# Kernel tuning notes

Hardware: AMD Instinct MI355X
Metric: run time of the kernel (lower is better)

## Reference

```python
import jax, jax.numpy as jnp
import numpy as np

PRUNE_N, PRUNE_M = 2, 4
RIA_A = 1.0
NUM_HEADS = 16
HEAD_DIM = 128
ROPE_THETA = 10000.0


def sparse_mask(W, scaler_row, perm):
    # RIA metric: |W|/colsum + |W|/rowsum, scaled by sqrt(scaler_row)**a
    absW = jnp.abs(W)
    metric = (absW / absW.sum(axis=0, keepdims=True)
              + absW / absW.sum(axis=1, keepdims=True))
    metric = metric * (jnp.sqrt(scaler_row)[None, :] ** RIA_A)
    Wm = metric @ perm                      # permute columns: [R, C]
    R, C = Wm.shape
    nb = C // PRUNE_M
    blocks = Wm.reshape(R, nb, PRUNE_M)
    # hard N:M mask: top-n per block of m
    _, idx = jax.lax.top_k(blocks, PRUNE_N)           # [R, nb, n]
    hard = jax.nn.one_hot(idx, PRUNE_M, dtype=Wm.dtype).sum(axis=-2)  # [R, nb, m]
    soft = jax.nn.softmax(blocks, axis=-1)
    hard = hard.reshape(R, C) @ perm.T
    soft = soft.reshape(R, C) @ perm.T
    # straight-through estimator
    return jax.lax.stop_gradient(hard - soft) + soft


def sparse_linear(x, W, b, scaler_row, perm):
    Wm = W * sparse_mask(W, scaler_row, perm)
    y = jnp.einsum('bsh,oh->bso', x, Wm)
    return y + b if b is not None else y


def rotate_half(x):
    x1, x2 = jnp.split(x, 2, axis=-1)
    return jnp.concatenate([-x2, x1], axis=-1)


def rope_tables(seq_len, dim, dtype):
    inv_freq = 1.0 / (ROPE_THETA ** (jnp.arange(0, dim, 2, dtype=jnp.float32) / dim))
    t = jnp.arange(seq_len, dtype=jnp.float32)
    freqs = jnp.outer(t, inv_freq)               # [S, dim/2]
    emb = jnp.concatenate([freqs, freqs], axis=-1)  # [S, dim]
    return jnp.cos(emb).astype(dtype), jnp.sin(emb).astype(dtype)


def setup_inputs() -> dict:
    key = jax.random.key(0)
    ks = jax.random.split(key, 16)
    H = 2048
    B, S = 2, 2048
    inp = {
        'hidden_states': jax.random.normal(ks[0], (B, S, H), jnp.float32) * 0.02,
        'Wq': jax.random.normal(ks[1], (H, H), jnp.float32) * 0.02,
        'bq': jax.random.normal(ks[2], (H,), jnp.float32) * 0.02,
        'Wk': jax.random.normal(ks[3], (H, H), jnp.float32) * 0.02,
        'bk': jax.random.normal(ks[4], (H,), jnp.float32) * 0.02,
        'Wv': jax.random.normal(ks[5], (H, H), jnp.float32) * 0.02,
        'bv': jax.random.normal(ks[6], (H,), jnp.float32) * 0.02,
        'Wo': jax.random.normal(ks[7], (H, H), jnp.float32) * 0.02,
        'sq': jax.random.uniform(ks[8], (H,), jnp.float32, 0.1, 1.0),
        'sk': jax.random.uniform(ks[9], (H,), jnp.float32, 0.1, 1.0),
        'sv': jax.random.uniform(ks[10], (H,), jnp.float32, 0.1, 1.0),
        'so': jax.random.uniform(ks[11], (H,), jnp.float32, 0.1, 1.0),
        'perm_qkv': jax.random.normal(ks[12], (H, H), jnp.float32) * 0.02,
        'perm_o': jax.random.normal(ks[13], (H, H), jnp.float32) * 0.02,
        'position_ids': jnp.broadcast_to(jnp.arange(S, dtype=jnp.int64), (B, S)),
    }
    return inp


def reference(hidden_states, Wq, bq, Wk, bk, Wv, bv, Wo,
              sq, sk, sv, so, perm_qkv, perm_o, position_ids):
    B, S, H = hidden_states.shape
    q = sparse_linear(hidden_states, Wq, bq, sq, perm_qkv)
    k = sparse_linear(hidden_states, Wk, bk, sk, perm_qkv)
    v = sparse_linear(hidden_states, Wv, bv, sv, perm_qkv)

    q = q.reshape(B, S, NUM_HEADS, HEAD_DIM).transpose(0, 2, 1, 3)  # [B,Hh,S,D]
    k = k.reshape(B, S, NUM_HEADS, HEAD_DIM).transpose(0, 2, 1, 3)
    v = v.reshape(B, S, NUM_HEADS, HEAD_DIM).transpose(0, 2, 1, 3)

    cos, sin = rope_tables(S, HEAD_DIM, q.dtype)
    c = cos[position_ids][:, None]  # [B,1,S,D]
    s = sin[position_ids][:, None]
    q = q * c + rotate_half(q) * s
    k = k * c + rotate_half(k) * s

    scores = jnp.einsum('bhqd,bhkd->bhqk', q, k) / np.sqrt(HEAD_DIM)
    causal = jnp.tril(jnp.ones((S, S), dtype=bool))
    scores = jnp.where(causal[None, None], scores, jnp.finfo(jnp.float32).min)
    attn = jax.nn.softmax(scores.astype(jnp.float32), axis=-1).astype(q.dtype)
    out = jnp.einsum('bhqk,bhkd->bhqd', attn, v)
    out = out.transpose(0, 2, 1, 3).reshape(B, S, H)
    out = sparse_linear(out, Wo, None, so, perm_o)
    return out
```

## Files before the change

### kernel.cpp

```cpp
#include <hip/hip_runtime.h>
#include <cstdint>
#include <cstddef>

typedef __attribute__((ext_vector_type(4))) float  f32x4;
typedef __attribute__((ext_vector_type(4))) int    i32x4;
typedef __attribute__((ext_vector_type(8))) short  s16x8;
typedef __attribute__((ext_vector_type(4))) short  s16x4;
typedef __attribute__((ext_vector_type(8))) __bf16 bf16x8;

struct Ptr4 { const float* p[4]; };

#define DEV __device__ __forceinline__

DEV unsigned short f2bf_u(float x) {
  unsigned u = __builtin_bit_cast(unsigned, x);
  u += 0x7fffu + ((u >> 16) & 1u);
  return (unsigned short)(u >> 16);
}
DEV float bfu2f(unsigned short u) {
  return __builtin_bit_cast(float, ((unsigned)u) << 16);
}
DEV bf16x8 ld_frag(const unsigned short* p) {
  s16x8 v = *(const s16x8*)p;
  return __builtin_bit_cast(bf16x8, v);
}
DEV f32x4 mfma16(bf16x8 a, bf16x8 b, f32x4 c) {
  return __builtin_amdgcn_mfma_f32_16x16x32_bf16(a, b, c, 0, 0, 0);
}
DEV void gload_lds16(const unsigned short* g, unsigned short* l) {
  __builtin_amdgcn_global_load_lds(
      (const __attribute__((address_space(1))) unsigned int*)g,
      (__attribute__((address_space(3))) unsigned int*)l, 16, 0, 0);
}

__global__ __launch_bounds__(256)
void k_rowsum(Ptr4 Ws, float* __restrict__ rowsums)
{
  const int row = blockIdx.x, mat = blockIdx.y, tid = threadIdx.x;
  const float* W = Ws.p[mat] + (size_t)row * 2048;
  float s = 0.f;
  #pragma unroll
  for (int p = 0; p < 2; ++p) {
    f32x4 v = *(const f32x4*)(W + p * 1024 + tid * 4);
    s += fabsf(v[0]) + fabsf(v[1]) + fabsf(v[2]) + fabsf(v[3]);
  }
  #pragma unroll
  for (int off = 1; off < 64; off <<= 1) s += __shfl_xor(s, off);
  __shared__ float red[4];
  if ((tid & 63) == 0) red[tid >> 6] = s;
  __syncthreads();
  if (tid == 0) rowsums[mat * 2048 + row] = red[0] + red[1] + red[2] + red[3];
}

__global__ __launch_bounds__(256)
void k_colsum_part(Ptr4 Ws, float* __restrict__ part)
{
  const int c = blockIdx.x * 256 + threadIdx.x;
  const int r0 = blockIdx.y * 64;
  const int mat = blockIdx.z;
  const float* W = Ws.p[mat];
  float s = 0.f;
  for (int rr = 0; rr < 64; ++rr) s += fabsf(W[(size_t)(r0 + rr) * 2048 + c]);
  part[((size_t)mat * 32 + blockIdx.y) * 2048 + c] = s;
}
__global__ __launch_bounds__(256)
void k_colsum_red(const float* __restrict__ part, float* __restrict__ colsums)
{
  const int gid = blockIdx.x * 256 + threadIdx.x;
  const int mat = gid >> 11, c = gid & 2047;
  float s = 0.f;
  #pragma unroll
  for (int j = 0; j < 32; ++j) s += part[((size_t)mat * 32 + j) * 2048 + c];
  colsums[gid] = s;
}

__global__ __launch_bounds__(256)
void k_metric(Ptr4 Ws, Ptr4 Ss, const float* __restrict__ rowsums,
              const float* __restrict__ colsums,
              unsigned short* __restrict__ mhi, unsigned short* __restrict__ mlo)
{
  const size_t idx4 = ((size_t)blockIdx.x * 256 + threadIdx.x) * 4;
  const int row = (int)(idx4 >> 11);
  const int c = (int)(idx4 & 2047);
  const int mat = row >> 11, rl = row & 2047;
  const float rs = rowsums[mat * 2048 + rl];
  f32x4 w  = *(const f32x4*)(Ws.p[mat] + (size_t)rl * 2048 + c);
  f32x4 cs = *(const f32x4*)(colsums + mat * 2048 + c);
  f32x4 sv = *(const f32x4*)(Ss.p[mat] + c);
  s16x4 hv, lv;
  #pragma unroll
  for (int j = 0; j < 4; ++j) {
    const float a = fabsf(w[j]);
    const float m = (a / cs[j] + a / rs) * sqrtf(sv[j]);
    const unsigned short hb = f2bf_u(m);
    hv[j] = (short)hb;
    lv[j] = (short)f2bf_u(m - bfu2f(hb));
  }
  *(s16x4*)(mhi + idx4) = hv;
  *(s16x4*)(mlo + idx4) = lv;
}

__global__ __launch_bounds__(256)
void k_perm_prep(const float* __restrict__ pq, const float* __restrict__ po,
                 unsigned short* __restrict__ thi_q, unsigned short* __restrict__ tlo_q,
                 unsigned short* __restrict__ thi_o, unsigned short* __restrict__ tlo_o,
                 unsigned short* __restrict__ pb_q, unsigned short* __restrict__ pb_o)
{
  __shared__ float T[64 * 65];
  const int which = blockIdx.z;
  const float* src = which ? po : pq;
  unsigned short* thi = which ? thi_o : thi_q;
  unsigned short* tlo = which ? tlo_o : tlo_q;
  unsigned short* pb  = which ? pb_o : pb_q;
  const int rb = blockIdx.y * 64, cb = blockIdx.x * 64, tid = threadIdx.x;
  #pragma unroll
  for (int i = 0; i < 4; ++i) {
    const int cc = i * 256 + tid;
    const int rowl = cc >> 4, c4 = (cc & 15) * 4;
    f32x4 v = *(const f32x4*)(src + (size_t)(rb + rowl) * 2048 + cb + c4);
    s16x4 pc;
    #pragma unroll
    for (int j = 0; j < 4; ++j) {
      T[rowl * 65 + c4 + j] = v[j];
      pc[j] = (short)f2bf_u(v[j]);
    }
    *(s16x4*)(pb + (size_t)(rb + rowl) * 2048 + cb + c4) = pc;
  }
  __syncthreads();
  #pragma unroll
  for (int i = 0; i < 4; ++i) {
    const int cc = i * 256 + tid;
    const int rowt = cc >> 4, c4 = (cc & 15) * 4;
    s16x4 hh, ll;
    #pragma unroll
    for (int j = 0; j < 4; ++j) {
      const float v = T[(c4 + j) * 65 + rowt];
      const unsigned short hb = f2bf_u(v);
      hh[j] = (short)hb;
      ll[j] = (short)f2bf_u(v - bfu2f(hb));
    }
    const size_t off = (size_t)(cb + rowt) * 2048 + rb + c4;
    *(s16x4*)(thi + off) = hh;
    *(s16x4*)(tlo + off) = ll;
  }
}

__global__ __launch_bounds__(256)
void k_cast_bf(const float* __restrict__ src, unsigned short* __restrict__ dst)
{
  const size_t i = ((size_t)blockIdx.x * 256 + threadIdx.x) * 8;
  f32x4 a = *(const f32x4*)(src + i);
  f32x4 b = *(const f32x4*)(src + i + 4);
  s16x8 o;
  #pragma unroll
  for (int j = 0; j < 4; ++j) o[j] = (short)f2bf_u(a[j]);
  #pragma unroll
  for (int j = 0; j < 4; ++j) o[4 + j] = (short)f2bf_u(b[j]);
  *(s16x8*)(dst + i) = o;
}

__global__ __launch_bounds__(256)
void k_rope_tab(float* __restrict__ ct, float* __restrict__ st)
{
  const int gid = blockIdx.x * 256 + threadIdx.x;
  const int s = gid >> 6, i = gid & 63;
  const float ex = (float)(2 * i) / 128.f;
  const float inv = 1.f / powf(10000.f, ex);
  const float f = (float)s * inv;
  ct[gid] = cosf(f);
  st[gid] = sinf(f);
}

__global__ __launch_bounds__(256)
void k_rope_reshape(const unsigned short* __restrict__ yqkv, const int* __restrict__ pos,
                    const float* __restrict__ ct, const float* __restrict__ st,
                    unsigned short* __restrict__ qo, unsigned short* __restrict__ ko)
{
  const int gid = blockIdx.x * 256 + threadIdx.x;
  const int d = gid & 127;
  const int s = (gid >> 7) & 2047;
  const int h = (gid >> 18) & 15;
  const int b = gid >> 22;
  const int t = b * 2048 + s;
  const int p = pos[t];
  const int dh = d & 63;
  const float cv = ct[p * 64 + dh], svv = st[p * 64 + dh];
  const size_t yb = (size_t)t * 6144 + h * 128;
  const float q0 = bfu2f(yqkv[yb + d]);
  const float k0 = bfu2f(yqkv[yb + 2048 + d]);
  const int pd = (d < 64) ? d + 64 : d - 64;
  float q1 = bfu2f(yqkv[yb + pd]);
  float k1 = bfu2f(yqkv[yb + 2048 + pd]);
  if (d < 64) { q1 = -q1; k1 = -k1; }
  const size_t o = ((size_t)(b * 16 + h) * 2048 + s) * 128 + d;
  qo[o] = f2bf_u(q0 * cv + q1 * svv);
  ko[o] = f2bf_u(k0 * cv + k1 * svv);
}

__global__ __launch_bounds__(256)
void k_vtrans(const unsigned short* __restrict__ yqkv, unsigned short* __restrict__ vt)
{
  __shared__ float T[64 * 129];
  const int st = blockIdx.x, bh = blockIdx.y, tid = threadIdx.x;
  const int b = bh >> 4, h = bh & 15;
  #pragma unroll
  for (int i = 0; i < 4; ++i) {
    const int c = i * 256 + tid;
    const int sl = c >> 4, d8 = (c & 15) * 8;
    s16x8 v = *(const s16x8*)(yqkv + (size_t)(b * 2048 + st * 64 + sl) * 6144 + 4096 + h * 128 + d8);
    #pragma unroll
    for (int j = 0; j < 8; ++j) T[sl * 129 + d8 + j] = bfu2f((unsigned short)v[j]);
  }
  __syncthreads();
  #pragma unroll
  for (int i = 0; i < 4; ++i) {
    const int c = i * 256 + tid;
    const int d = c >> 3, s8 = (c & 7) * 8;
    s16x8 o;
    #pragma unroll
    for (int j = 0; j < 8; ++j) o[j] = (short)f2bf_u(T[(s8 + j) * 129 + d]);
    *(s16x8*)(vt + ((size_t)bh * 128 + d) * 2048 + st * 64 + s8) = o;
  }
}

template<int MODE, int SPLIT>
__global__ __launch_bounds__(256)
void gemm_bt(const unsigned short* __restrict__ Ahi, const unsigned short* __restrict__ Alo,
             const unsigned short* __restrict__ Bhi_1, const unsigned short* __restrict__ Blo_1,
             const unsigned short* __restrict__ Bhi_2, const unsigned short* __restrict__ Blo_2,
             int bswitch,
             float* __restrict__ Cf, unsigned short* __restrict__ Cb,
             Ptr4 aux, int M, int N, int K)
{
  __shared__ alignas(16) unsigned short As[2 * 4096];
  __shared__ alignas(16) unsigned short Bs[2 * 4096];
  const int tid = threadIdx.x;
  const int lane = tid & 63, wid = tid >> 6;
  const int wm = wid >> 1, wn = wid & 1;
  const int r = lane & 15, g = lane >> 4;
  const int mbase = blockIdx.y * 128;
  const int nbase = blockIdx.x * 128;
  const int KT = K >> 5;
  (void)M;
  const unsigned short* Bhi = (mbase >= bswitch) ? Bhi_2 : Bhi_1;
  const unsigned short* Blo = (mbase >= bswitch) ? Blo_2 : Blo_1;

  const f32x4 zero = {0.f, 0.f, 0.f, 0.f};
  f32x4 acc[4][4];
  #pragma unroll
  for (int i = 0; i < 4; ++i) {
    #pragma unroll
    for (int j = 0; j < 4; ++j) acc[i][j] = zero;
  }

  const int srl = lane >> 2;
  const int sch = lane & 3;

  auto issue_tile = [&](int kt, int buf) {
    const size_t kb = (size_t)kt * 32;
    #pragma unroll
    for (int i = 0; i < 2; ++i) {
      const int rbase = wid * 32 + i * 16;
      const int rloc = rbase + srl;
      const int sc = ((sch ^ ((rloc >> 1) & 3)) << 3);
      const size_t ga = (size_t)(mbase + rloc) * K + kb + sc;
      const size_t gb = (size_t)(nbase + rloc) * K + kb + sc;
      gload_lds16(Ahi + ga, &As[buf * 4096 + rbase * 32]);
      gload_lds16(Bhi + gb, &Bs[buf * 4096 + rbase * 32]);
      if (SPLIT) {
        gload_lds16(Alo + ga, &As[4096 + rbase * 32]);
        gload_lds16(Blo + gb, &Bs[4096 + rbase * 32]);
      }
    }
  };

  if (SPLIT) {
    issue_tile(0, 0);
    for (int kt = 0; kt < KT; ++kt) {
      __syncthreads();

      bf16x8 ah[4], bfr[4], al[4], bl[4];
      #pragma unroll
      for (int mi = 0; mi < 4; ++mi) {
        const int arow = wm * 64 + mi * 16 + r;
        const int sw = ((g ^ ((arow >> 1) & 3)) << 3);
        ah[mi] = ld_frag(&As[arow * 32 + sw]);
        al[mi] = ld_frag(&As[4096 + arow * 32 + sw]);
      }
      #pragma unroll
      for (int ni = 0; ni < 4; ++ni) {
        const int brow = wn * 64 + ni * 16 + r;
        const int sw = ((g ^ ((brow >> 1) & 3)) << 3);
        bfr[ni] = ld_frag(&Bs[brow * 32 + sw]);
        bl[ni] = ld_frag(&Bs[4096 + brow * 32 + sw]);
      }
      __syncthreads();
      if (kt + 1 < KT) issue_tile(kt + 1, 0);

      #pragma unroll
      for (int mi = 0; mi < 4; ++mi) {
        #pragma unroll
        for (int ni = 0; ni < 4; ++ni) {
          acc[mi][ni] = mfma16(al[mi], bfr[ni], acc[mi][ni]);
          acc[mi][ni] = mfma16(ah[mi], bl[ni], acc[mi][ni]);
          acc[mi][ni] = mfma16(ah[mi], bfr[ni], acc[mi][ni]);
        }
      }
    }
  } else {
    issue_tile(0, 0);
    int cur = 0;
    for (int kt = 0; kt < KT; ++kt) {
      __syncthreads();
      if (kt + 1 < KT) issue_tile(kt + 1, cur ^ 1);

      bf16x8 ah[4], bfr[4];
      #pragma unroll
      for (int mi = 0; mi < 4; ++mi) {
        const int arow = wm * 64 + mi * 16 + r;
        ah[mi] = ld_frag(&As[cur * 4096 + arow * 32 + ((g ^ ((arow >> 1) & 3)) << 3)]);
      }
      #pragma unroll
      for (int ni = 0; ni < 4; ++ni) {
        const int brow = wn * 64 + ni * 16 + r;
        bfr[ni] = ld_frag(&Bs[cur * 4096 + brow * 32 + ((g ^ ((brow >> 1) & 3)) << 3)]);
      }
      #pragma unroll
      for (int mi = 0; mi < 4; ++mi) {
        #pragma unroll
        for (int ni = 0; ni < 4; ++ni)
          acc[mi][ni] = mfma16(ah[mi], bfr[ni], acc[mi][ni]);
      }
      cur ^= 1;
    }
  }

  #pragma unroll
  for (int mi = 0; mi < 4; ++mi) {
    #pragma unroll
    for (int ni = 0; ni < 4; ++ni) {
      const int row0 = mbase + wm * 64 + mi * 16 + g * 4;
      const int col  = nbase + wn * 64 + ni * 16 + r;
      if (MODE == 0) {
        #pragma unroll
        for (int e = 0; e < 4; ++e)
          Cf[(size_t)(row0 + e) * N + col] = acc[mi][ni][e];
      } else if (MODE == 1) {
        const float* wsrc = aux.p[row0 >> 11];
        #pragma unroll
        for (int e = 0; e < 4; ++e) {
          const float mval = wsrc[(size_t)((row0 + e) & 2047) * 2048 + col];
          Cb[(size_t)(row0 + e) * N + col] = f2bf_u(acc[mi][ni][e] * mval);
        }
      } else if (MODE == 2) {
        const float* bp = aux.p[col >> 11];
        const float bb = bp[col & 2047];
        #pragma unroll
        for (int e = 0; e < 4; ++e)
          Cb[(size_t)(row0 + e) * N + col] = f2bf_u(acc[mi][ni][e] + bb);
      } else {
        const int ii = r & 3;
        #pragma unroll
        for (int e = 0; e < 4; ++e) {
          const float v  = acc[mi][ni][e];
          const float v1 = __shfl_xor(v, 1);
          const float v2 = __shfl_xor(v, 2);
          const float v3 = __shfl_xor(v, 3);
          int cnt = 0;
          { const int j = ii ^ 1; cnt += (v1 > v) || (v1 == v && j < ii); }
          { const int j = ii ^ 2; cnt += (v2 > v) || (v2 == v && j < ii); }
          { const int j = ii ^ 3; cnt += (v3 > v) || (v3 == v && j < ii); }
          Cb[(size_t)(row0 + e) * N + col] =
              (cnt < 2) ? (unsigned short)0x3F80 : (unsigned short)0;
        }
      }
    }
  }
}

__global__ __launch_bounds__(256)
void attn_fa(const unsigned short* __restrict__ Qh, const unsigned short* __restrict__ Kh,
             const unsigned short* __restrict__ Vt, unsigned short* __restrict__ Out)
{
  __shared__ alignas(16) unsigned short Ks[64 * 128];
  __shared__ alignas(16) unsigned short Vs[128 * 64];
  __shared__ alignas(16) unsigned short Ps[4][1024];
  const int tid = threadIdx.x, lane = tid & 63, wid = tid >> 6;
  const int r = lane & 15, g = lane >> 4;
  const int pair = blockIdx.x, bh = blockIdx.y;
  const int b = bh >> 4, h = bh & 15;
  const f32x4 zero = {0.f, 0.f, 0.f, 0.f};

  i32x4 kr[4], vr[4];
  auto issue_kv = [&](int kvt) {
    #pragma unroll
    for (int i = 0; i < 4; ++i) {
      const int c = i * 256 + tid;
      {
        const int row = c >> 4, slot = c & 15;
        kr[i] = *(const i32x4*)(Kh + ((size_t)bh * 2048 + kvt * 64 + row) * 128 + slot * 8);
      }
      {
        const int row = c >> 3, slot = c & 7;
        vr[i] = *(const i32x4*)(Vt + ((size_t)bh * 128 + row) * 2048 + kvt * 64 + slot * 8);
      }
    }
  };

  for (int half = 0; half < 2; ++half) {
    const int qt = half ? (31 - pair) : pair;
    const int qrow0 = qt * 64 + wid * 16;

    bf16x8 qf[4];
    {
      const unsigned short* qp = Qh + ((size_t)bh * 2048 + qrow0 + r) * 128;
      #pragma unroll
      for (int ks = 0; ks < 4; ++ks) qf[ks] = ld_frag(qp + ks * 32 + g * 8);
    }
    f32x4 oacc[8];
    #pragma unroll
    for (int i = 0; i < 8; ++i) oacc[i] = zero;
    float m_run[4] = {-1e30f, -1e30f, -1e30f, -1e30f};
    float l_run[4] = {0.f, 0.f, 0.f, 0.f};

    issue_kv(0);
    for (int kvt = 0; kvt <= qt; ++kvt) {
      __syncthreads();
      #pragma unroll
      for (int i = 0; i < 4; ++i) {
        const int c = i * 256 + tid;
        {
          const int row = c >> 4, slot = c & 15;
          *(i32x4*)&Ks[row * 128 + ((slot ^ (row & 7)) << 3)] = kr[i];
        }
        {
          const int row = c >> 3, slot = c & 7;
          *(i32x4*)&Vs[row * 64 + ((slot ^ (row & 7)) << 3)] = vr[i];
        }
      }
      __syncthreads();
      if (kvt < qt) issue_kv(kvt + 1);

      f32x4 sc[4];
      #pragma unroll
      for (int ni = 0; ni < 4; ++ni) sc[ni] = zero;
      #pragma unroll
      for (int ks = 0; ks < 4; ++ks) {
        const int slot = (ks << 2) | g;
        #pragma unroll
        for (int ni = 0; ni < 4; ++ni) {
          const int krow = ni * 16 + r;
          bf16x8 kf = ld_frag(&Ks[krow * 128 + ((slot ^ (krow & 7)) << 3)]);
          sc[ni] = mfma16(qf[ks], kf, sc[ni]);
        }
      }
      const float sscale = 0.08838834764831845f;
      if (kvt == qt) {
        #pragma unroll
        for (int ni = 0; ni < 4; ++ni) {
          const int kvg = kvt * 64 + ni * 16 + r;
          #pragma unroll
          for (int e = 0; e < 4; ++e) {
            const int qg = qrow0 + g * 4 + e;
            const float s = sc[ni][e] * sscale;
            sc[ni][e] = (kvg > qg) ? -1e30f : s;
          }
        }
      } else {
        #pragma unroll
        for (int ni = 0; ni < 4; ++ni) {
          #pragma unroll
          for (int e = 0; e < 4; ++e) sc[ni][e] *= sscale;
        }
      }
      float corr[4];
      #pragma unroll
      for (int e = 0; e < 4; ++e) {
        float mx = fmaxf(fmaxf(sc[0][e], sc[1][e]), fmaxf(sc[2][e], sc[3][e]));
        mx = fmaxf(mx, __shfl_xor(mx, 1));
        mx = fmaxf(mx, __shfl_xor(mx, 2));
        mx = fmaxf(mx, __shfl_xor(mx, 4));
        mx = fmaxf(mx, __shfl_xor(mx, 8));
        const float mn = fmaxf(m_run[e], mx);
        corr[e] = exp2f((m_run[e] - mn) * 1.4426950408889634f);
        m_run[e] = mn;
      }
      float psum[4] = {0.f, 0.f, 0.f, 0.f};
      #pragma unroll
      for (int ni = 0; ni < 4; ++ni) {
        #pragma unroll
        for (int e = 0; e < 4; ++e) {
          const float p = exp2f((sc[ni][e] - m_run[e]) * 1.4426950408889634f);
          sc[ni][e] = p;
          psum[e] += p;
        }
      }
      #pragma unroll
      for (int e = 0; e < 4; ++e) {
        float s = psum[e];
        s += __shfl_xor(s, 1);
        s += __shfl_xor(s, 2);
        s += __shfl_xor(s, 4);
        s += __shfl_xor(s, 8);
        l_run[e] = l_run[e] * corr[e] + s;
      }
      #pragma unroll
      for (int nf = 0; nf < 8; ++nf) {
        #pragma unroll
        for (int e = 0; e < 4; ++e) oacc[nf][e] *= corr[e];
      }
      #pragma unroll
      for (int ni = 0; ni < 4; ++ni) {
        #pragma unroll
        for (int e = 0; e < 4; ++e) {
          const int prow = g * 4 + e;
          const int col = ni * 16 + r;
          const int slot = col >> 3;
          Ps[wid][prow * 64 + ((slot ^ (prow & 7)) << 3) + (col & 7)] = f2bf_u(sc[ni][e]);
        }
      }
      #pragma unroll
      for (int ks = 0; ks < 2; ++ks) {
        const int slot = (ks << 2) | g;
        bf16x8 pf = ld_frag(&Ps[wid][r * 64 + ((slot ^ (r & 7)) << 3)]);
        #pragma unroll
        for (int nf = 0; nf < 8; ++nf) {
          const int vrow = nf * 16 + r;
          bf16x8 vf = ld_frag(&Vs[vrow * 64 + ((slot ^ (vrow & 7)) << 3)]);
          oacc[nf] = mfma16(pf, vf, oacc[nf]);
        }
      }
    }
    #pragma unroll
    for (int e = 0; e < 4; ++e) {
      const float inv = 1.f / l_run[e];
      const int qg = qrow0 + g * 4 + e;
      #pragma unroll
      for (int nf = 0; nf < 8; ++nf) {
        const int d = nf * 16 + r;
        Out[((size_t)(b * 2048 + qg)) * 2048 + h * 128 + d] = f2bf_u(oacc[nf][e] * inv);
      }
    }
  }
}

extern "C" void kernel_launch(void* const* d_in, const int* in_sizes, int n_in,
                              void* d_out, int out_size, void* d_ws, size_t ws_size,
                              hipStream_t stream)
{
  (void)in_sizes; (void)n_in; (void)out_size; (void)ws_size;
  const float* hid   = (const float*)d_in[0];
  const float* Wq    = (const float*)d_in[1];
  const float* bq    = (const float*)d_in[2];
  const float* Wk    = (const float*)d_in[3];
  const float* bk    = (const float*)d_in[4];
  const float* Wv    = (const float*)d_in[5];
  const float* bv    = (const float*)d_in[6];
  const float* Wo    = (const float*)d_in[7];
  const float* sq    = (const float*)d_in[8];
  const float* sk    = (const float*)d_in[9];
  const float* sv    = (const float*)d_in[10];
  const float* so    = (const float*)d_in[11];
  const float* permq = (const float*)d_in[12];
  const float* permo = (const float*)d_in[13];
  const int* pos     = (const int*)d_in[14];
  float* out = (float*)d_out;
  char* ws = (char*)d_ws;

  constexpr size_t OFF_ROWS = 0;
  constexpr size_t OFF_COLS = OFF_ROWS + (size_t)4 * 2048 * 4;
  constexpr size_t OFF_PART = OFF_COLS + (size_t)4 * 2048 * 4;
  constexpr size_t OFF_COS  = OFF_PART + (size_t)4 * 32 * 2048 * 4;
  constexpr size_t OFF_SIN  = OFF_COS + (size_t)2048 * 64 * 4;
  constexpr size_t SZ_PERM  = (size_t)2048 * 2048 * 2;
  constexpr size_t OFF_A    = OFF_SIN + (size_t)2048 * 64 * 4;
  constexpr size_t OFF_PTQH = OFF_A;
  constexpr size_t OFF_PTQL = OFF_PTQH + SZ_PERM;
  constexpr size_t OFF_PTOH = OFF_PTQL + SZ_PERM;
  constexpr size_t OFF_PTOL = OFF_PTOH + SZ_PERM;
  constexpr size_t OFF_PBQ  = OFF_PTOL + SZ_PERM;
  constexpr size_t OFF_PBO  = OFF_PBQ + SZ_PERM;
  constexpr size_t SZ_M8    = (size_t)8192 * 2048 * 2;
  constexpr size_t OFF_B    = OFF_PBO + SZ_PERM;
  constexpr size_t OFF_C    = OFF_B + SZ_M8;
  constexpr size_t OFF_D    = OFF_C + SZ_M8;
  constexpr size_t OFF_E    = OFF_D + SZ_M8;

  float* rowsums = (float*)(ws + OFF_ROWS);
  float* colsums = (float*)(ws + OFF_COLS);
  float* part    = (float*)(ws + OFF_PART);
  float* cost    = (float*)(ws + OFF_COS);
  float* sint    = (float*)(ws + OFF_SIN);
  unsigned short* ptqh = (unsigned short*)(ws + OFF_PTQH);
  unsigned short* ptql = (unsigned short*)(ws + OFF_PTQL);
  unsigned short* ptoh = (unsigned short*)(ws + OFF_PTOH);
  unsigned short* ptol = (unsigned short*)(ws + OFF_PTOL);
  unsigned short* pbq  = (unsigned short*)(ws + OFF_PBQ);
  unsigned short* pbo  = (unsigned short*)(ws + OFF_PBO);
  unsigned short* mhi  = (unsigned short*)(ws + OFF_B);
  unsigned short* mlo  = (unsigned short*)(ws + OFF_C);
  unsigned short* hard = (unsigned short*)(ws + OFF_D);
  unsigned short* wfin = (unsigned short*)(ws + OFF_E);
  unsigned short* yqkv = (unsigned short*)(ws + OFF_B);
  unsigned short* qhb  = (unsigned short*)(ws + OFF_A);
  unsigned short* khb  = (unsigned short*)(ws + OFF_A + 2 * SZ_PERM);
  unsigned short* vtg  = (unsigned short*)(ws + OFF_A + 4 * SZ_PERM);
  unsigned short* xbf  = (unsigned short*)(ws + OFF_D);
  unsigned short* att  = (unsigned short*)(ws + OFF_D + SZ_M8 / 2);

  Ptr4 Wptrs{{Wq, Wk, Wv, Wo}};
  Ptr4 Sptrs{{sq, sk, sv, so}};
  Ptr4 BiasP{{bq, bk, bv, nullptr}};
  Ptr4 NoAux{{nullptr, nullptr, nullptr, nullptr}};
  constexpr int NOSW = 1 << 30;

  k_rowsum<<<dim3(2048, 4), 256, 0, stream>>>(Wptrs, rowsums);
  k_colsum_part<<<dim3(8, 32, 4), 256, 0, stream>>>(Wptrs, part);
  k_colsum_red<<<32, 256, 0, stream>>>(part, colsums);
  k_metric<<<16384, 256, 0, stream>>>(Wptrs, Sptrs, rowsums, colsums, mhi, mlo);
  k_perm_prep<<<dim3(32, 32, 2), 256, 0, stream>>>(permq, permo, ptqh, ptql, ptoh, ptol, pbq, pbo);
  gemm_bt<3, 1><<<dim3(16, 64), 256, 0, stream>>>(mhi, mlo, ptqh, ptql, ptoh, ptol, 6144,
                                                  nullptr, hard, NoAux, 8192, 2048, 2048);
  gemm_bt<1, 0><<<dim3(16, 64), 256, 0, stream>>>(hard, nullptr, pbq, nullptr, pbo, nullptr, 6144,
                                                  nullptr, wfin, Wptrs, 8192, 2048, 2048);
  k_cast_bf<<<4096, 256, 0, stream>>>(hid, xbf);
  gemm_bt<2, 0><<<dim3(48, 32), 256, 0, stream>>>(xbf, nullptr, wfin, nullptr, wfin, nullptr, NOSW,
                                                  nullptr, yqkv, BiasP, 4096, 6144, 2048);
  k_rope_tab<<<512, 256, 0, stream>>>(cost, sint);
  k_rope_reshape<<<32768, 256, 0, stream>>>(yqkv, pos, cost, sint, qhb, khb);
  k_vtrans<<<dim3(32, 32), 256, 0, stream>>>(yqkv, vtg);
  attn_fa<<<dim3(16, 32), 256, 0, stream>>>(qhb, khb, vtg, att);
  gemm_bt<0, 0><<<dim3(16, 32), 256, 0, stream>>>(att, nullptr, wfin + (size_t)6144 * 2048, nullptr,
                                                  wfin + (size_t)6144 * 2048, nullptr, NOSW,
                                                  out, nullptr, NoAux, 4096, 2048, 2048);
}
```

Before: 663.2 us.

## Vectorize RoPE kernel, add XCD-aware block swizzle, and MFMA priority hints

```diff
diff --git a/kernel.cpp b/kernel.cpp
--- a/kernel.cpp
+++ b/kernel.cpp
@@ -31,6 +31,10 @@
   __builtin_amdgcn_global_load_lds(
       (const __attribute__((address_space(1))) unsigned int*)g,
       (__attribute__((address_space(3))) unsigned int*)l, 16, 0, 0);
+}
+DEV int xcd_swizzle(int bid, int nwg) {
+  const int q8 = nwg >> 3;
+  return (bid & 7) * q8 + (bid >> 3);
 }
 
 __global__ __launch_bounds__(256)
@@ -177,24 +181,34 @@
                     unsigned short* __restrict__ qo, unsigned short* __restrict__ ko)
 {
   const int gid = blockIdx.x * 256 + threadIdx.x;
-  const int d = gid & 127;
-  const int s = (gid >> 7) & 2047;
-  const int h = (gid >> 18) & 15;
-  const int b = gid >> 22;
+  const int d8 = gid & 15;
+  const int s = (gid >> 4) & 2047;
+  const int h = (gid >> 15) & 15;
+  const int b = gid >> 19;
   const int t = b * 2048 + s;
   const int p = pos[t];
-  const int dh = d & 63;
-  const float cv = ct[p * 64 + dh], svv = st[p * 64 + dh];
   const size_t yb = (size_t)t * 6144 + h * 128;
-  const float q0 = bfu2f(yqkv[yb + d]);
-  const float k0 = bfu2f(yqkv[yb + 2048 + d]);
-  const int pd = (d < 64) ? d + 64 : d - 64;
-  float q1 = bfu2f(yqkv[yb + pd]);
-  float k1 = bfu2f(yqkv[yb + 2048 + pd]);
-  if (d < 64) { q1 = -q1; k1 = -k1; }
-  const size_t o = ((size_t)(b * 16 + h) * 2048 + s) * 128 + d;
-  qo[o] = f2bf_u(q0 * cv + q1 * svv);
-  ko[o] = f2bf_u(k0 * cv + k1 * svv);
+  s16x8 qv = *(const s16x8*)(yqkv + yb + d8 * 8);
+  s16x8 qp = *(const s16x8*)(yqkv + yb + (d8 ^ 8) * 8);
+  s16x8 kv = *(const s16x8*)(yqkv + yb + 2048 + d8 * 8);
+  s16x8 kp = *(const s16x8*)(yqkv + yb + 2048 + (d8 ^ 8) * 8);
+  const int dh0 = (d8 & 7) * 8;
+  const float sgn = (d8 < 8) ? -1.f : 1.f;
+  s16x8 qo8, ko8;
+  #pragma unroll
+  for (int j = 0; j < 8; ++j) {
+    const float cv = ct[p * 64 + dh0 + j];
+    const float sv = st[p * 64 + dh0 + j];
+    const float q0 = bfu2f((unsigned short)qv[j]);
+    const float k0 = bfu2f((unsigned short)kv[j]);
+    const float q1 = sgn * bfu2f((unsigned short)qp[j]);
+    const float k1 = sgn * bfu2f((unsigned short)kp[j]);
+    qo8[j] = (short)f2bf_u(q0 * cv + q1 * sv);
+    ko8[j] = (short)f2bf_u(k0 * cv + k1 * sv);
+  }
+  const size_t o = ((size_t)(b * 16 + h) * 2048 + s) * 128 + d8 * 8;
+  *(s16x8*)(qo + o) = qo8;
+  *(s16x8*)(ko + o) = ko8;
 }
 
 __global__ __launch_bounds__(256)
@@ -238,8 +252,11 @@
   const int lane = tid & 63, wid = tid >> 6;
   const int wm = wid >> 1, wn = wid & 1;
   const int r = lane & 15, g = lane >> 4;
-  const int mbase = blockIdx.y * 128;
-  const int nbase = blockIdx.x * 128;
+  const int nwg = gridDim.x * gridDim.y;
+  const int sw = xcd_swizzle(blockIdx.y * gridDim.x + blockIdx.x, nwg);
+  const int tx = sw % gridDim.x, ty = sw / gridDim.x;
+  const int mbase = ty * 128;
+  const int nbase = tx * 128;
   const int KT = K >> 5;
   (void)M;
   const unsigned short* Bhi = (mbase >= bswitch) ? Bhi_2 : Bhi_1;
@@ -283,16 +300,16 @@
       #pragma unroll
       for (int mi = 0; mi < 4; ++mi) {
         const int arow = wm * 64 + mi * 16 + r;
-        const int sw = ((g ^ ((arow >> 1) & 3)) << 3);
-        ah[mi] = ld_frag(&As[arow * 32 + sw]);
-        al[mi] = ld_frag(&As[4096 + arow * 32 + sw]);
+        const int sw2 = ((g ^ ((arow >> 1) & 3)) << 3);
+        ah[mi] = ld_frag(&As[arow * 32 + sw2]);
+        al[mi] = ld_frag(&As[4096 + arow * 32 + sw2]);
       }
       #pragma unroll
       for (int ni = 0; ni < 4; ++ni) {
         const int brow = wn * 64 + ni * 16 + r;
-        const int sw = ((g ^ ((brow >> 1) & 3)) << 3);
-        bfr[ni] = ld_frag(&Bs[brow * 32 + sw]);
-        bl[ni] = ld_frag(&Bs[4096 + brow * 32 + sw]);
+        const int sw2 = ((g ^ ((brow >> 1) & 3)) << 3);
+        bfr[ni] = ld_frag(&Bs[brow * 32 + sw2]);
+        bl[ni] = ld_frag(&Bs[4096 + brow * 32 + sw2]);
       }
       __syncthreads();
       if (kt + 1 < KT) issue_tile(kt + 1, 0);
@@ -387,7 +404,8 @@
   __shared__ alignas(16) unsigned short Ps[4][1024];
   const int tid = threadIdx.x, lane = tid & 63, wid = tid >> 6;
   const int r = lane & 15, g = lane >> 4;
-  const int pair = blockIdx.x, bh = blockIdx.y;
+  const int sw = xcd_swizzle(blockIdx.y * gridDim.x + blockIdx.x, gridDim.x * gridDim.y);
+  const int pair = sw % 16, bh = sw / 16;
   const int b = bh >> 4, h = bh & 15;
   const f32x4 zero = {0.f, 0.f, 0.f, 0.f};
 
@@ -444,6 +462,7 @@
       f32x4 sc[4];
       #pragma unroll
       for (int ni = 0; ni < 4; ++ni) sc[ni] = zero;
+      __builtin_amdgcn_s_setprio(1);
       #pragma unroll
       for (int ks = 0; ks < 4; ++ks) {
         const int slot = (ks << 2) | g;
@@ -454,6 +473,7 @@
           sc[ni] = mfma16(qf[ks], kf, sc[ni]);
         }
       }
+      __builtin_amdgcn_s_setprio(0);
       const float sscale = 0.08838834764831845f;
       if (kvt == qt) {
         #pragma unroll
@@ -519,6 +539,7 @@
           Ps[wid][prow * 64 + ((slot ^ (prow & 7)) << 3) + (col & 7)] = f2bf_u(sc[ni][e]);
         }
       }
+      __builtin_amdgcn_s_setprio(1);
       #pragma unroll
       for (int ks = 0; ks < 2; ++ks) {
         const int slot = (ks << 2) | g;
@@ -530,6 +551,7 @@
           oacc[nf] = mfma16(pf, vf, oacc[nf]);
         }
       }
+      __builtin_amdgcn_s_setprio(0);
     }
     #pragma unroll
     for (int e = 0; e < 4; ++e) {
@@ -627,7 +649,7 @@
   gemm_bt<2, 0><<<dim3(48, 32), 256, 0, stream>>>(xbf, nullptr, wfin, nullptr, wfin, nullptr, NOSW,
                                                   nullptr, yqkv, BiasP, 4096, 6144, 2048);
   k_rope_tab<<<512, 256, 0, stream>>>(cost, sint);
-  k_rope_reshape<<<32768, 256, 0, stream>>>(yqkv, pos, cost, sint, qhb, khb);
+  k_rope_reshape<<<4096, 256, 0, stream>>>(yqkv, pos, cost, sint, qhb, khb);
   k_vtrans<<<dim3(32, 32), 256, 0, stream>>>(yqkv, vtg);
   attn_fa<<<dim3(16, 32), 256, 0, stream>>>(qhb, khb, vtg, att);
   gemm_bt<0, 0><<<dim3(16, 32), 256, 0, stream>>>(att, nullptr, wfin + (size_t)6144 * 2048, nullptr,
```

New measurement: 649.8 us. 1.02x faster.
